# Optimization experiments

Hardware: AMD Instinct MI355X
Metric: run time of the kernel (lower is better)

Reference implementation:

```python
import jax, jax.numpy as jnp
import numpy as np

# Fixed rendering constants (non-tensor forward args of the module)
THETA_RANGE = (0.0, float(np.pi) / 2.0)
PHI_RANGE = (-float(np.pi) / 2.0, float(np.pi) / 2.0)
R_RANGE = (0.5, 2.5)
C_LIGHT = 1.0          # speed of light (normalized units)
DELTA_T = 0.03125      # time-bin width -> step = C_LIGHT*DELTA_T = (2.0/64)
SCALING_MODIFIER = 1.0
USE_OCCLUSION = True
SH_C0 = 0.28209479177387814
G = 2048


def quat_to_rotmat(q):
    # q: [G,4] (w,x,y,z), unnormalized -> [G,3,3]
    q = q / (jnp.linalg.norm(q, axis=-1, keepdims=True) + 1e-12)
    w, x, y, z = q[:, 0], q[:, 1], q[:, 2], q[:, 3]
    R = jnp.stack([
        1 - 2 * (y * y + z * z), 2 * (x * y - w * z), 2 * (x * z + w * y),
        2 * (x * y + w * z), 1 - 2 * (x * x + z * z), 2 * (y * z - w * x),
        2 * (x * z - w * y), 2 * (y * z + w * x), 1 - 2 * (x * x + y * y),
    ], axis=-1)
    return R.reshape(-1, 3, 3)


def setup_inputs() -> dict:
    key = jax.random.key(0)
    k1, k2, k3, k4, k5 = jax.random.split(key, 5)
    # Gaussians clustered in front of the sensor (camera at origin, +z hemisphere)
    gaussian_means = jax.random.normal(k1, (G, 3), jnp.float32) * 0.5 + jnp.array([0.0, 0.0, 1.5], jnp.float32)
    gaussian_scales = jax.random.normal(k2, (G, 3), jnp.float32) * 0.3 - 2.5   # log-scales -> exp ~ 0.08
    gaussian_rotations = jax.random.normal(k3, (G, 4), jnp.float32)
    gaussian_opacities = jax.random.normal(k4, (G, 1), jnp.float32)
    gaussian_features = jax.random.normal(k5, (G, 3), jnp.float32) * 0.5
    camera_pos = jnp.zeros((3,), jnp.float32)
    return {
        "gaussian_means": gaussian_means,
        "gaussian_scales": gaussian_scales,
        "gaussian_rotations": gaussian_rotations,
        "gaussian_opacities": gaussian_opacities,
        "gaussian_features": gaussian_features,
        "camera_pos": camera_pos,
        "num_theta": 32,
        "num_phi": 32,
        "num_r": 64,
    }


def reference(gaussian_means, gaussian_scales, gaussian_rotations,
              gaussian_opacities, gaussian_features, camera_pos,
              num_theta, num_phi, num_r):
    # --- ray construction (module wrapper) ---
    theta = jnp.linspace(THETA_RANGE[0], THETA_RANGE[1], num_theta)
    phi = jnp.linspace(PHI_RANGE[0], PHI_RANGE[1], num_phi)
    tg, pg = jnp.meshgrid(theta, phi, indexing='ij')           # [nt,np]
    th, ph = tg.reshape(-1), pg.reshape(-1)                    # [R]
    dirs = jnp.stack([jnp.sin(th) * jnp.cos(ph),
                      jnp.sin(th) * jnp.sin(ph),
                      jnp.cos(th)], axis=1)                    # [R,3]
    t = jnp.linspace(R_RANGE[0], R_RANGE[1], num_r)            # [S]

    # --- Gaussian parameter activation ---
    scales = jnp.exp(gaussian_scales) * SCALING_MODIFIER       # [G,3]
    Rm = quat_to_rotmat(gaussian_rotations)                    # [G,3,3]
    inv_s2 = 1.0 / (scales * scales)                           # [G,3]
    prec = jnp.einsum('gij,gj,gkj->gik', Rm, inv_s2, Rm)       # Sigma^{-1} [G,3,3]
    opac = jax.nn.sigmoid(gaussian_opacities[:, 0])            # [G]
    albedo = jnp.mean(jnp.clip(SH_C0 * gaussian_features + 0.5, 0.0, None), axis=-1)  # [G]

    # --- per-(sample,ray,gaussian) Mahalanobis quadratic, factored in t ---
    # (o + t d - mu)^T P (o + t d - mu) = A[r,g] t^2 + B[r,g] t + Cq[g]
    om = camera_pos[None, :] - gaussian_means                  # [G,3]
    A = jnp.einsum('rd,gde,re->rg', dirs, prec, dirs)          # [R,G]
    B = 2.0 * jnp.einsum('rd,gde,ge->rg', dirs, prec, om)      # [R,G]
    Cq = jnp.einsum('gd,gde,ge->g', om, prec, om)              # [G]
    t2 = t * t
    quad = (A[None] * t2[:, None, None]
            + B[None] * t[:, None, None]
            + Cq[None, None])                                  # [S,R,G]
    w = opac[None, None, :] * jnp.exp(-0.5 * quad)             # [S,R,G]
    density = jnp.sum(w, axis=-1)                              # [S,R]
    rho = jnp.sum(w * albedo[None, None, :], axis=-1)          # [S,R]

    # --- sequential transmittance accumulation along the ray ---
    step = C_LIGHT * DELTA_T
    acc = jnp.cumsum(density * step, axis=0)
    acc_excl = jnp.concatenate([jnp.zeros_like(acc[:1]), acc[:-1]], axis=0)
    transmittance = jnp.exp(-acc_excl)                         # [S,R]
    rho_density = rho * transmittance if USE_OCCLUSION else rho

    # --- module post-processing ---
    result = rho_density.reshape(num_r, num_theta, num_phi)
    result = result / (t[:, None, None] ** 2 + 1e-8) * jnp.sin(tg)[None]
    dtheta = (THETA_RANGE[1] - THETA_RANGE[0]) / num_theta
    dphi = (PHI_RANGE[1] - PHI_RANGE[0]) / num_phi
    pred_histogram = jnp.sum(result, axis=(1, 2)) * dtheta * dphi
    return result, pred_histogram
```

## Files before the change

### kernel.cpp

```cpp
#include <hip/hip_runtime.h>
#include <math.h>

#define G_N   2048
#define NT    32
#define NP    32
#define NR    64
#define NRAY  (NT * NP)
#define PLANE 8196

__global__ __launch_bounds__(512) void k_main(
    const float* __restrict__ means, const float* __restrict__ scales,
    const float* __restrict__ rots, const float* __restrict__ opacs,
    const float* __restrict__ feats, const float* __restrict__ cam,
    float* __restrict__ out) {
  __shared__ float coef[4 * PLANE];
  __shared__ float red[2][8][256];

  const int tid  = threadIdx.x;
  const int ray0 = blockIdx.x * 4;
  const int ti   = ray0 >> 5;
  const int pj0  = ray0 & 31;

  const float dth = (float)(M_PI / 2.0 / (NT - 1));
  const float dph = (float)(M_PI / (NP - 1));
  float sth, cth;
  sincosf((float)ti * dth, &sth, &cth);
  const float dz = cth, dzz = dz * dz;

  float dX[4], dY[4], dXX[4], dYY[4], dXY[4], dXZ[4], dYZ[4];
  #pragma unroll
  for (int r = 0; r < 4; ++r) {
    float ph = (float)(-M_PI / 2.0) + (float)(pj0 + r) * dph;
    float sp, cp;
    sincosf(ph, &sp, &cp);
    float dx = sth * cp, dy = sth * sp;
    dX[r] = dx; dY[r] = dy;
    dXX[r] = dx * dx; dYY[r] = dy * dy;
    dXY[r] = 2.f * dx * dy; dXZ[r] = 2.f * dx * dz; dYZ[r] = 2.f * dy * dz;
  }

  const float cx = cam[0], cy = cam[1], cz = cam[2];
  const float c      = -0.7213475204444817f;
  const float l2e    = 1.4426950408889634f;
  const float n2l2e  = -2.8853900817779268f;
  const float SH_C0  = 0.28209479177387814f;

  #pragma unroll
  for (int i = 0; i < G_N / 512; ++i) {
    int g = tid + i * 512;
    float i0 = __builtin_amdgcn_exp2f(n2l2e * scales[3*g+0]);
    float i1 = __builtin_amdgcn_exp2f(n2l2e * scales[3*g+1]);
    float i2 = __builtin_amdgcn_exp2f(n2l2e * scales[3*g+2]);

    float qw = rots[4*g+0], qx = rots[4*g+1], qy = rots[4*g+2], qz = rots[4*g+3];
    float inv = __builtin_amdgcn_rsqf(qw*qw + qx*qx + qy*qy + qz*qz);
    qw *= inv; qx *= inv; qy *= inv; qz *= inv;

    float R00 = 1.f - 2.f*(qy*qy + qz*qz), R01 = 2.f*(qx*qy - qw*qz), R02 = 2.f*(qx*qz + qw*qy);
    float R10 = 2.f*(qx*qy + qw*qz), R11 = 1.f - 2.f*(qx*qx + qz*qz), R12 = 2.f*(qy*qz - qw*qx);
    float R20 = 2.f*(qx*qz - qw*qy), R21 = 2.f*(qy*qz + qw*qx), R22 = 1.f - 2.f*(qx*qx + qy*qy);

    float p00 = c*(R00*R00*i0 + R01*R01*i1 + R02*R02*i2);
    float p11 = c*(R10*R10*i0 + R11*R11*i1 + R12*R12*i2);
    float p22 = c*(R20*R20*i0 + R21*R21*i1 + R22*R22*i2);
    float p01 = c*(R00*R10*i0 + R01*R11*i1 + R02*R12*i2);
    float p02 = c*(R00*R20*i0 + R01*R21*i1 + R02*R22*i2);
    float p12 = c*(R10*R20*i0 + R11*R21*i1 + R12*R22*i2);

    float ox = cx - means[3*g+0], oy = cy - means[3*g+1], oz = cz - means[3*g+2];
    float Px = p00*ox + p01*oy + p02*oz;
    float Py = p01*ox + p11*oy + p12*oz;
    float Pz = p02*ox + p12*oy + p22*oz;
    float Cq = ox*Px + oy*Py + oz*Pz;

    float u = __builtin_amdgcn_exp2f(-l2e * opacs[g]);
    float Cf = Cq - __builtin_amdgcn_logf(1.0f + u);

    float a0 = fmaxf(SH_C0*feats[3*g+0] + 0.5f, 0.f);
    float a1 = fmaxf(SH_C0*feats[3*g+1] + 0.5f, 0.f);
    float a2 = fmaxf(SH_C0*feats[3*g+2] + 0.5f, 0.f);
    float alb = (a0 + a1 + a2) * (1.0f/3.0f);

    #pragma unroll
    for (int r = 0; r < 4; ++r) {
      float A = p00*dXX[r] + p11*dYY[r] + p22*dzz + p01*dXY[r] + p02*dXZ[r] + p12*dYZ[r];
      float B = 2.f * (Px*dX[r] + Py*dY[r] + Pz*dz);
      *(float4*)&coef[r * PLANE + g * 4] = make_float4(A, B, Cf, alb);
    }
  }
  __syncthreads();

  const int lane = tid & 63;
  const int wv   = tid >> 6;
  const int r    = lane >> 4;
  const int tt   = lane & 15;
  const float tstep = 2.0f / 63.0f;
  const float t0 = 0.5f + (float)tt * tstep;
  const float t1 = t0 + 16.f * tstep;
  const float t2 = t0 + 32.f * tstep;
  const float t3 = t0 + 48.f * tstep;

  const float4* basep = (const float4*)&coef[r * PLANE] + wv * (G_N / 8);
  float d0 = 0.f, d1 = 0.f, d2 = 0.f, d3 = 0.f;
  float h0 = 0.f, h1 = 0.f, h2 = 0.f, h3 = 0.f;
  #pragma unroll 8
  for (int g = 0; g < G_N / 8; ++g) {
    float4 e = basep[g];
    float q0 = fmaf(fmaf(e.x, t0, e.y), t0, e.z);
    float q1 = fmaf(fmaf(e.x, t1, e.y), t1, e.z);
    float q2 = fmaf(fmaf(e.x, t2, e.y), t2, e.z);
    float q3 = fmaf(fmaf(e.x, t3, e.y), t3, e.z);
    float x0 = __builtin_amdgcn_exp2f(q0);
    float x1 = __builtin_amdgcn_exp2f(q1);
    float x2 = __builtin_amdgcn_exp2f(q2);
    float x3 = __builtin_amdgcn_exp2f(q3);
    d0 += x0; h0 = fmaf(x0, e.w, h0);
    d1 += x1; h1 = fmaf(x1, e.w, h1);
    d2 += x2; h2 = fmaf(x2, e.w, h2);
    d3 += x3; h3 = fmaf(x3, e.w, h3);
  }

  red[0][wv][r*64 + tt     ] = d0;  red[1][wv][r*64 + tt     ] = h0;
  red[0][wv][r*64 + tt + 16] = d1;  red[1][wv][r*64 + tt + 16] = h1;
  red[0][wv][r*64 + tt + 32] = d2;  red[1][wv][r*64 + tt + 32] = h2;
  red[0][wv][r*64 + tt + 48] = d3;  red[1][wv][r*64 + tt + 48] = h3;
  __syncthreads();

  if (tid < 256) {
    const int rr = tid >> 6;
    const int t  = tid & 63;
    int idx = rr * 64 + t;
    float D  = ((red[0][0][idx] + red[0][1][idx]) + (red[0][2][idx] + red[0][3][idx]))
             + ((red[0][4][idx] + red[0][5][idx]) + (red[0][6][idx] + red[0][7][idx]));
    float Rh = ((red[1][0][idx] + red[1][1][idx]) + (red[1][2][idx] + red[1][3][idx]))
             + ((red[1][4][idx] + red[1][5][idx]) + (red[1][6][idx] + red[1][7][idx]));
    const float step = 1.0f * 0.03125f;
    float s = D * step;
    float inc = s;
    #pragma unroll
    for (int off = 1; off < 64; off <<= 1) {
      float v = __shfl_up(inc, off, 64);
      if (t >= off) inc += v;
    }
    float excl = inc - s;
    float T = __builtin_amdgcn_exp2f(-1.4426950408889634f * excl);
    float tv = 0.5f + (float)t * tstep;
    float res = Rh * T / (tv * tv + 1e-8f) * sth;
    out[t * NRAY + ray0 + rr] = res;
  }
}

__global__ __launch_bounds__(256) void k_hist(const float* __restrict__ res,
                                              float* __restrict__ hist) {
  const int t = blockIdx.x;
  const int tid = threadIdx.x;
  float s = 0.f;
  #pragma unroll
  for (int rr = tid; rr < NRAY; rr += 256) s += res[t * NRAY + rr];
  #pragma unroll
  for (int off = 32; off > 0; off >>= 1) s += __shfl_down(s, off, 64);
  __shared__ float sm[4];
  if ((tid & 63) == 0) sm[tid >> 6] = s;
  __syncthreads();
  if (tid == 0) {
    const float dtdp = (float)((M_PI / 2.0 / NT) * (M_PI / NP));
    hist[t] = ((sm[0] + sm[1]) + (sm[2] + sm[3])) * dtdp;
  }
}

extern "C" void kernel_launch(void* const* d_in, const int* in_sizes, int n_in,
                              void* d_out, int out_size, void* d_ws, size_t ws_size,
                              hipStream_t stream) {
  const float* means  = (const float*)d_in[0];
  const float* scales = (const float*)d_in[1];
  const float* rots   = (const float*)d_in[2];
  const float* opacs  = (const float*)d_in[3];
  const float* feats  = (const float*)d_in[4];
  const float* cam    = (const float*)d_in[5];

  float* out = (float*)d_out;

  k_main<<<NRAY / 4, 512, 0, stream>>>(means, scales, rots, opacs, feats, cam, out);
  k_hist<<<NR,       256, 0, stream>>>(out, out + NR * NRAY);
}
```

Measured before the change: 95.27 us.

## Cull negligible Gaussians per ray via compaction before the exp-accumulation loop

```diff
diff --git a/kernel.cpp b/kernel.cpp
--- a/kernel.cpp
+++ b/kernel.cpp
@@ -7,6 +7,7 @@
 #define NR    64
 #define NRAY  (NT * NP)
 #define PLANE 8196
+#define QCULL -30.0f
 
 __global__ __launch_bounds__(512) void k_main(
     const float* __restrict__ means, const float* __restrict__ scales,
@@ -15,11 +16,17 @@
     float* __restrict__ out) {
   __shared__ float coef[4 * PLANE];
   __shared__ float red[2][8][256];
+  __shared__ int   nact[4];
 
   const int tid  = threadIdx.x;
+  const int lane = tid & 63;
+  const int wv   = tid >> 6;
   const int ray0 = blockIdx.x * 4;
   const int ti   = ray0 >> 5;
   const int pj0  = ray0 & 31;
+
+  if (tid < 4) nact[tid] = 0;
+  __syncthreads();
 
   const float dth = (float)(M_PI / 2.0 / (NT - 1));
   const float dph = (float)(M_PI / (NP - 1));
@@ -73,7 +80,7 @@
     float Pz = p02*ox + p12*oy + p22*oz;
     float Cq = ox*Px + oy*Py + oz*Pz;
 
-    float u = __builtin_amdgcn_exp2f(-l2e * opacs[g]);
+    float u  = __builtin_amdgcn_exp2f(-l2e * opacs[g]);
     float Cf = Cq - __builtin_amdgcn_logf(1.0f + u);
 
     float a0 = fmaxf(SH_C0*feats[3*g+0] + 0.5f, 0.f);
@@ -85,27 +92,35 @@
     for (int r = 0; r < 4; ++r) {
       float A = p00*dXX[r] + p11*dYY[r] + p22*dzz + p01*dXY[r] + p02*dXZ[r] + p12*dYZ[r];
       float B = 2.f * (Px*dX[r] + Py*dY[r] + Pz*dz);
-      *(float4*)&coef[r * PLANE + g * 4] = make_float4(A, B, Cf, alb);
+      float tstar = fminf(2.5f, fmaxf(0.5f, -B / (2.f * A)));
+      float qm = fmaf(fmaf(A, tstar, B), tstar, Cf);
+      bool keep = qm > QCULL;
+      unsigned long long m = __ballot(keep);
+      int base;
+      if (lane == 0) base = atomicAdd(&nact[r], __popcll(m));
+      base = __shfl(base, 0, 64);
+      if (keep) {
+        int slot = base + __popcll(m & ((1ull << lane) - 1ull));
+        *(float4*)&coef[r * PLANE + slot * 4] = make_float4(A, B, Cf, alb);
+      }
     }
   }
   __syncthreads();
 
-  const int lane = tid & 63;
-  const int wv   = tid >> 6;
-  const int r    = lane >> 4;
-  const int tt   = lane & 15;
+  const int r  = lane >> 4;
+  const int ts = lane & 15;
   const float tstep = 2.0f / 63.0f;
-  const float t0 = 0.5f + (float)tt * tstep;
+  const float t0 = 0.5f + (float)ts * tstep;
   const float t1 = t0 + 16.f * tstep;
   const float t2 = t0 + 32.f * tstep;
   const float t3 = t0 + 48.f * tstep;
 
-  const float4* basep = (const float4*)&coef[r * PLANE] + wv * (G_N / 8);
+  const int n = nact[r];
+  const float4* basep = (const float4*)&coef[r * PLANE];
   float d0 = 0.f, d1 = 0.f, d2 = 0.f, d3 = 0.f;
   float h0 = 0.f, h1 = 0.f, h2 = 0.f, h3 = 0.f;
-  #pragma unroll 8
-  for (int g = 0; g < G_N / 8; ++g) {
-    float4 e = basep[g];
+  for (int j = wv; j < n; j += 8) {
+    float4 e = basep[j];
     float q0 = fmaf(fmaf(e.x, t0, e.y), t0, e.z);
     float q1 = fmaf(fmaf(e.x, t1, e.y), t1, e.z);
     float q2 = fmaf(fmaf(e.x, t2, e.y), t2, e.z);
@@ -120,10 +135,10 @@
     d3 += x3; h3 = fmaf(x3, e.w, h3);
   }
 
-  red[0][wv][r*64 + tt     ] = d0;  red[1][wv][r*64 + tt     ] = h0;
-  red[0][wv][r*64 + tt + 16] = d1;  red[1][wv][r*64 + tt + 16] = h1;
-  red[0][wv][r*64 + tt + 32] = d2;  red[1][wv][r*64 + tt + 32] = h2;
-  red[0][wv][r*64 + tt + 48] = d3;  red[1][wv][r*64 + tt + 48] = h3;
+  red[0][wv][r*64 + ts     ] = d0;  red[1][wv][r*64 + ts     ] = h0;
+  red[0][wv][r*64 + ts + 16] = d1;  red[1][wv][r*64 + ts + 16] = h1;
+  red[0][wv][r*64 + ts + 32] = d2;  red[1][wv][r*64 + ts + 32] = h2;
+  red[0][wv][r*64 + ts + 48] = d3;  red[1][wv][r*64 + ts + 48] = h3;
   __syncthreads();
 
   if (tid < 256) {
```

Measured after the change: 88.70 us. -6.9%, faster.
